# Optimization experiments

Measured on AMD Instinct MI355X. Metric: run time of the kernel, lower is better.

The kernel has to match this reference:

```python
import jax, jax.numpy as jnp
import numpy as np
from jax import lax

B, L_IN, D, D_INNER = 4, 1024, 512, 512
H, DK = 8, 64
WIN = [4, 4, 4]
INNER_SIZE = 5   # temporal intra-level neighborhood size
SEM_K = 32       # opt.semantic_node: topk per level for semantic mask
N_LAYER = 2


def _build_temporal_mask(input_size, window_size, inner_size):
    # faithful port of Encoder.get_mask (Pyraformer-Naive mask)
    all_size = [input_size]
    for w in window_size:
        all_size.append(all_size[-1] // w)
    L = sum(all_size)
    m = np.zeros((L, L), dtype=np.float32)
    iw = inner_size // 2
    starts = [sum(all_size[:i]) for i in range(len(all_size))]
    for li, n in enumerate(all_size):
        st = starts[li]
        for i in range(st, st + n):
            m[i, max(i - iw, st):min(i + iw + 1, st + n)] = 1
    for li in range(1, len(all_size)):
        st = starts[li]
        prev = all_size[li - 1]
        w = window_size[li - 1]
        for i in range(st, st + all_size[li]):
            ls = st - prev + (i - st) * w
            rs = st if i == st + all_size[li] - 1 else st - prev + (i - st + 1) * w
            m[i, ls:rs] = 1
            m[ls:rs, i] = 1
    return (1 - m).astype(bool), all_size

TMASK_NP, ALL_SIZE = _build_temporal_mask(L_IN, WIN, INNER_SIZE)
L_TOT = sum(ALL_SIZE)  # 1360


def _ln(x, g, b, eps):
    mu = jnp.mean(x, axis=-1, keepdims=True)
    var = jnp.mean(jnp.square(x - mu), axis=-1, keepdims=True)
    return (x - mu) * lax.rsqrt(var + eps) * g + b


def _mha(x, Wq, Wk, Wv, fcW, fcb, g, b, mask):
    # post-norm MHA (normalize_before=False), dropout disabled (eval)
    Bq, L, _ = x.shape
    q = (x @ Wq).reshape(Bq, L, H, DK)
    k = (x @ Wk).reshape(Bq, L, H, DK)
    v = (x @ Wv).reshape(Bq, L, H, DK)
    a = jnp.einsum('bqhd,bkhd->bhqk', q, k) / np.float32(DK ** 0.5)
    a = jnp.where(mask, -jnp.inf, a)
    p = jax.nn.softmax(a, axis=-1)
    o = jnp.einsum('bhqk,bkhd->bqhd', p, v).reshape(Bq, L, H * DK)
    return _ln(o @ fcW + fcb + x, g, b, 1e-6)


def _semantic_mask(x):
    # get_semantic_mask: per-level cosine similarity, mask topk-most-similar within each level
    nrm = jnp.linalg.norm(x, axis=-1, keepdims=True)
    xn = x / jnp.maximum(nrm, 1e-8)
    sim = jnp.einsum('bid,bjd->bij', xn, xn)
    Bq = x.shape[0]
    mask = jnp.zeros((Bq, L_TOT, L_TOT), dtype=bool)
    bidx = jnp.arange(Bq)[:, None, None]
    start = 0
    for n in ALL_SIZE:
        k = min(n, SEM_K)
        blk = sim[:, start:start + n, start:start + n]
        idx = lax.top_k(blk, k)[1]              # [B, n, k]
        ridx = jnp.arange(n)[None, :, None]
        bm = jnp.zeros((Bq, n, n), dtype=bool).at[bidx, ridx, idx].set(True)
        mask = mask.at[:, start:start + n, start:start + n].set(bm)
        start += n
    return mask


def _bottleneck(x, dW, db, cW, cb, uW, ub, g, b):
    t = jnp.transpose(x @ dW + db, (0, 2, 1))  # [B, d_inner, L]
    outs = []
    for i in range(len(WIN)):
        t = lax.conv_general_dilated(t, cW[i], (WIN[i],), 'VALID',
                                     dimension_numbers=('NCH', 'OIH', 'NCH')) + cb[i][None, :, None]
        t = t / np.float32(np.sqrt(1.0 + 1e-5))  # eval BatchNorm with identity running stats
        t = jax.nn.elu(t)
        outs.append(t)
    pyr = jnp.transpose(jnp.concatenate(outs, axis=2), (0, 2, 1)) @ uW + ub
    return _ln(jnp.concatenate([x, pyr], axis=1), g, b, 1e-5)


def _forward(x_enc, down_W, down_b, conv_W, conv_b, up_W, up_b, bc_ln_g, bc_ln_b,
             attn_Wq, attn_Wk, attn_Wv, attn_fcW, attn_fcb, attn_ln_g, attn_ln_b,
             ffn_W1, ffn_b1, ffn_W2, ffn_b2, ffn_ln_g, ffn_ln_b):
    tmask = jnp.asarray(TMASK_NP)[None, None]  # [1,1,Lt,Lt]
    x = _bottleneck(x_enc, down_W, down_b, conv_W, conv_b, up_W, up_b, bc_ln_g, bc_ln_b)
    for l in range(N_LAYER):
        res = x
        t_out = _mha(x, attn_Wq[l, 0], attn_Wk[l, 0], attn_Wv[l, 0], attn_fcW[l, 0],
                     attn_fcb[l, 0], attn_ln_g[l, 0], attn_ln_b[l, 0], tmask)
        smask = _semantic_mask(x)[:, None]     # [B,1,Lt,Lt]
        s_out = _mha(x, attn_Wq[l, 1], attn_Wk[l, 1], attn_Wv[l, 1], attn_fcW[l, 1],
                     attn_fcb[l, 1], attn_ln_g[l, 1], attn_ln_b[l, 1], smask)
        x = (t_out + s_out + res) / 3.0
        res = x
        h = jax.nn.relu(x @ ffn_W1[l] + ffn_b1[l])
        x = _ln(h @ ffn_W2[l] + ffn_b2[l] + res, ffn_ln_g[l], ffn_ln_b[l], 1e-6)
    return x


def setup_inputs() -> dict:
    key = jax.random.key(0)
    ks = jax.random.split(key, 16)
    s = 0.02
    inp = {
        'x_enc': jax.random.normal(ks[0], (B, L_IN, D), jnp.float32),
        'down_W': jax.random.normal(ks[1], (D, D_INNER), jnp.float32) * s,
        'down_b': jnp.zeros((D_INNER,), jnp.float32),
        'conv_W': jax.random.normal(ks[2], (3, D_INNER, D_INNER, WIN[0]), jnp.float32) * s,
        'conv_b': jnp.zeros((3, D_INNER), jnp.float32),
        'up_W': jax.random.normal(ks[3], (D_INNER, D), jnp.float32) * s,
        'up_b': jnp.zeros((D,), jnp.float32),
        'bc_ln_g': jnp.ones((D,), jnp.float32),
        'bc_ln_b': jnp.zeros((D,), jnp.float32),
        'attn_Wq': jax.random.normal(ks[4], (N_LAYER, 2, D, H * DK), jnp.float32) * s,
        'attn_Wk': jax.random.normal(ks[5], (N_LAYER, 2, D, H * DK), jnp.float32) * s,
        'attn_Wv': jax.random.normal(ks[6], (N_LAYER, 2, D, H * DK), jnp.float32) * s,
        'attn_fcW': jax.random.normal(ks[7], (N_LAYER, 2, H * DK, D), jnp.float32) * s,
        'attn_fcb': jnp.zeros((N_LAYER, 2, D), jnp.float32),
        'attn_ln_g': jnp.ones((N_LAYER, 2, D), jnp.float32),
        'attn_ln_b': jnp.zeros((N_LAYER, 2, D), jnp.float32),
        'ffn_W1': jax.random.normal(ks[8], (N_LAYER, D, D_INNER), jnp.float32) * s,
        'ffn_b1': jnp.zeros((N_LAYER, D_INNER), jnp.float32),
        'ffn_W2': jax.random.normal(ks[9], (N_LAYER, D_INNER, D), jnp.float32) * s,
        'ffn_b2': jnp.zeros((N_LAYER, D), jnp.float32),
        'ffn_ln_g': jnp.ones((N_LAYER, D), jnp.float32),
        'ffn_ln_b': jnp.zeros((N_LAYER, D), jnp.float32),
    }
    return inp


def reference(x_enc, down_W, down_b, conv_W, conv_b, up_W, up_b, bc_ln_g, bc_ln_b,
              attn_Wq, attn_Wk, attn_Wv, attn_fcW, attn_fcb, attn_ln_g, attn_ln_b,
              ffn_W1, ffn_b1, ffn_W2, ffn_b2, ffn_ln_g, ffn_ln_b):
    return _forward(x_enc, down_W, down_b, conv_W, conv_b, up_W, up_b, bc_ln_g, bc_ln_b,
                    attn_Wq, attn_Wk, attn_Wv, attn_fcW, attn_fcb, attn_ln_g, attn_ln_b,
                    ffn_W1, ffn_b1, ffn_W2, ffn_b2, ffn_ln_g, ffn_ln_b)
```

## Files before the change

kernel.cpp:

```cpp
#include <hip/hip_runtime.h>
#include <float.h>
#include <math.h>
#include <stdint.h>

#define LT 1360
#define BB 4
#define DM 512
#define NHH 8
#define NBLE 2785280
#define MBW 24
#define QSCALE 0.18033688f

typedef __attribute__((ext_vector_type(8))) short short8;
typedef __attribute__((ext_vector_type(4))) float f32x4;
typedef unsigned long long u64;

__device__ __forceinline__ ushort f2b(float x){
    uint32_t u = __float_as_uint(x);
    return (ushort)((u + 0x7fffu + ((u >> 16) & 1u)) >> 16);
}
__device__ __forceinline__ float b2f(ushort u){
    return __uint_as_float(((uint32_t)u) << 16);
}
__device__ __forceinline__ float ex2(float x){
    float r;
    asm("v_exp_f32 %0, %1" : "=v"(r) : "v"(x));
    return r;
}
__device__ __forceinline__ uint32_t pkbf(float lo, float hi){
    uint32_t r;
    asm("v_cvt_pk_bf16_f32 %0, %1, %2" : "=v"(r) : "v"(lo), "v"(hi));
    return r;
}

#define SG0 0
#define SG1 1048576
#define SG2 (SG1 + 65536)
#define SG3 (SG2 + 4096)
#define SBT (SG3 + 256)

__device__ __forceinline__ void blk_info(int i, int& bi, int& st, int& n){
    if (i < 1024){ bi = 0; st = 0;    n = 1024; }
    else if (i < 1280){ bi = 1; st = 1024; n = 256; }
    else if (i < 1344){ bi = 2; st = 1280; n = 64; }
    else { bi = 3; st = 1344; n = 16; }
}

__global__ __launch_bounds__(256)
void build_tidx(int* __restrict__ idx, int* __restrict__ cnt){
    int i = blockIdx.x * 256 + threadIdx.x;
    if (i >= LT) return;
    int bi, st, n; blk_info(i, bi, st, n);
    int c = 0; int* row = idx + i * 12;
    int lo = (i - 2 > st) ? i - 2 : st;
    int hi = (i + 2 < st + n - 1) ? i + 2 : st + n - 1;
    for (int j = lo; j <= hi; j++) row[c++] = j;
    if (bi < 3) row[c++] = st + n + (i - st) / 4;
    if (bi > 0){
        int stc = st - n * 4;
        int base = stc + (i - st) * 4;
        for (int t = 0; t < 4; t++) row[c++] = base + t;
    }
    cnt[i] = c;
    for (int t = c; t < 12; t++) row[t] = 0;
}

__global__ __launch_bounds__(256)
void wtrans(const float* __restrict__ W, ushort* __restrict__ Wt, int K, int N, long dstStride){
    int mat = blockIdx.z;
    const float* Ws = W + (size_t)mat * K * N;
    ushort* Wd = Wt + (size_t)mat * dstStride;
    int k0 = blockIdx.y << 6, n0 = blockIdx.x << 6;
    __shared__ ushort t[64][72];
    int tid = threadIdx.x;
    #pragma unroll
    for (int p = 0; p < 4; p++){
        int idx = tid + (p << 8);
        int r = idx >> 4, c4 = (idx & 15) << 2;
        float4 v = *(const float4*)(Ws + (size_t)(k0 + r) * N + n0 + c4);
        t[c4+0][r] = f2b(v.x); t[c4+1][r] = f2b(v.y);
        t[c4+2][r] = f2b(v.z); t[c4+3][r] = f2b(v.w);
    }
    __syncthreads();
    #pragma unroll
    for (int p = 0; p < 4; p++){
        int idx = tid + (p << 8);
        int r = idx >> 4, c4 = (idx & 15) << 2;
        *(uint2*)&Wd[(size_t)(n0 + r) * K + k0 + c4] = *(uint2*)&t[r][c4];
    }
}

__global__ __launch_bounds__(256)
void wconv(const float* __restrict__ cw, ushort* __restrict__ wt){
    int conv = blockIdx.y;
// ... 447 lines not shown
    *(uint4*)&Bl[srow][sc8] = vbl;
    __syncthreads();
    for (int k0 = 0; k0 < 512; k0 += 32){
        bool nx = (k0 + 32 < 512);
        if (nx){
            vah = *(const uint4*)(pAh + k0 + 32);
            val = *(const uint4*)(pAl + k0 + 32);
            vbh = *(const uint4*)(pBh + k0 + 32);
            vbl = *(const uint4*)(pBl + k0 + 32);
        }
        __builtin_amdgcn_s_setprio(1);
        short8 ah0 = *(const short8*)&Ah[wr + l15][quad << 3];
        short8 ah1 = *(const short8*)&Ah[wr + 16 + l15][quad << 3];
        short8 al0 = *(const short8*)&Al[wr + l15][quad << 3];
        short8 al1 = *(const short8*)&Al[wr + 16 + l15][quad << 3];
        short8 bh0 = *(const short8*)&Bh[wc + l15][quad << 3];
        short8 bh1 = *(const short8*)&Bh[wc + 16 + l15][quad << 3];
        short8 bl0 = *(const short8*)&Bl[wc + l15][quad << 3];
        short8 bl1 = *(const short8*)&Bl[wc + 16 + l15][quad << 3];
        acc[0][0] = __builtin_amdgcn_mfma_f32_16x16x32_bf16(ah0, bh0, acc[0][0], 0, 0, 0);
        acc[0][0] = __builtin_amdgcn_mfma_f32_16x16x32_bf16(ah0, bl0, acc[0][0], 0, 0, 0);
        acc[0][0] = __builtin_amdgcn_mfma_f32_16x16x32_bf16(al0, bh0, acc[0][0], 0, 0, 0);
        acc[0][1] = __builtin_amdgcn_mfma_f32_16x16x32_bf16(ah0, bh1, acc[0][1], 0, 0, 0);
        acc[0][1] = __builtin_amdgcn_mfma_f32_16x16x32_bf16(ah0, bl1, acc[0][1], 0, 0, 0);
        acc[0][1] = __builtin_amdgcn_mfma_f32_16x16x32_bf16(al0, bh1, acc[0][1], 0, 0, 0);
        acc[1][0] = __builtin_amdgcn_mfma_f32_16x16x32_bf16(ah1, bh0, acc[1][0], 0, 0, 0);
        acc[1][0] = __builtin_amdgcn_mfma_f32_16x16x32_bf16(ah1, bl0, acc[1][0], 0, 0, 0);
        acc[1][0] = __builtin_amdgcn_mfma_f32_16x16x32_bf16(al1, bh0, acc[1][0], 0, 0, 0);
        acc[1][1] = __builtin_amdgcn_mfma_f32_16x16x32_bf16(ah1, bh1, acc[1][1], 0, 0, 0);
        acc[1][1] = __builtin_amdgcn_mfma_f32_16x16x32_bf16(ah1, bl1, acc[1][1], 0, 0, 0);
        acc[1][1] = __builtin_amdgcn_mfma_f32_16x16x32_bf16(al1, bh1, acc[1][1], 0, 0, 0);
        __builtin_amdgcn_s_setprio(0);
        if (nx){
            __syncthreads();
            *(uint4*)&Ah[srow][sc8] = vah;
            *(uint4*)&Al[srow][sc8] = val;
            *(uint4*)&Bh[srow][sc8] = vbh;
            *(uint4*)&Bl[srow][sc8] = vbl;
            __syncthreads();
        }
    }
    #pragma unroll
    for (int mi = 0; mi < 2; mi++){
        #pragma unroll
        for (int r = 0; r < 4; r++){
            int row = gm + wr + (mi << 4) + (quad << 2) + r;
            if (row < n){
                #pragma unroll
                for (int ni = 0; ni < 2; ni++){
                    int col = gn + wc + (ni << 4) + l15;
                    if (col < n) Cb[(size_t)row * n + col] = acc[mi][ni][r];
                }
            }
        }
    }
}

__global__ __launch_bounds__(256)
void pcat_copy(const float* __restrict__ C1, const float* __restrict__ C2,
               const float* __restrict__ C3, float* __restrict__ PC){
    int idx = blockIdx.x * 256 + threadIdx.x;
    int d = idx & 511;
    int r = (idx >> 9) % 336;
    int b = idx / (336 * 512);
    float v;
    if (r < 256)       v = C1[(((size_t)b * 256 + r) << 9) + d];
    else if (r < 320)  v = C2[(((size_t)b * 64 + (r - 256)) << 9) + d];
    else               v = C3[(((size_t)b * 16 + (r - 320)) << 9) + d];
    PC[idx] = v;
}

__global__ __launch_bounds__(256)
void xenc_copy(const float* __restrict__ xe, float* __restrict__ dst){
    int idx = blockIdx.x * 256 + threadIdx.x;
    int d = idx & 511;
    int l = (idx >> 9) & 1023;
    int b = idx >> 19;
    dst[(((size_t)b * LT + l) << 9) + d] = xe[idx];
}

__global__ __launch_bounds__(256)
void ln_kernel(const float* __restrict__ in, const float* __restrict__ g,
               const float* __restrict__ bta, float* __restrict__ out,
               ushort* __restrict__ ob, float eps){
    int wid = threadIdx.x >> 6, lane = threadIdx.x & 63;
    int row = blockIdx.x * 4 + wid;
    const float* p = in + ((size_t)row << 9);
    float vals[8]; float s = 0.f, s2 = 0.f;
    #pragma unroll
    for (int t = 0; t < 8; t++){
        float v = p[lane + t * 64]; vals[t] = v; s += v; s2 += v * v;
    }
    #pragma unroll
    for (int off = 32; off; off >>= 1){
        s  += __shfl_xor(s,  off, 64);
        s2 += __shfl_xor(s2, off, 64);
    }
    float mu = s * (1.f / 512.f);
    float var = s2 * (1.f / 512.f) - mu * mu;
    float r = rsqrtf(var + eps);
    float* q = out + ((size_t)row << 9);
    ushort* qb = ob ? ob + ((size_t)row << 9) : nullptr;
    #pragma unroll
    for (int t = 0; t < 8; t++){
        int c = lane + t * 64;
        float v = (vals[t] - mu) * r * g[c] + bta[c];
        q[c] = v;
        if (qb) qb[c] = f2b(v);
    }
}

__global__ __launch_bounds__(256)
void ln2_add3(const float* __restrict__ in0, const float* __restrict__ in1,
              const float* __restrict__ g0, const float* __restrict__ b0,
              const float* __restrict__ g1, const float* __restrict__ b1,
              float* __restrict__ X, ushort* __restrict__ ob, float eps){
    int wid = threadIdx.x >> 6, lane = threadIdx.x & 63;
    int row = blockIdx.x * 4 + wid;
    const float* p0 = in0 + ((size_t)row << 9);
    const float* p1 = in1 + ((size_t)row << 9);
    float v0[8], v1[8];
    float s0 = 0.f, q0 = 0.f, s1 = 0.f, q1 = 0.f;
    #pragma unroll
    for (int t = 0; t < 8; t++){
        float a = p0[lane + t * 64]; v0[t] = a; s0 += a; q0 += a * a;
        float c = p1[lane + t * 64]; v1[t] = c; s1 += c; q1 += c * c;
    }
    #pragma unroll
    for (int off = 32; off; off >>= 1){
        s0 += __shfl_xor(s0, off, 64);
        q0 += __shfl_xor(q0, off, 64);
        s1 += __shfl_xor(s1, off, 64);
        q1 += __shfl_xor(q1, off, 64);
    }
    float mu0 = s0 * (1.f / 512.f);
    float r0 = rsqrtf(q0 * (1.f / 512.f) - mu0 * mu0 + eps);
    float mu1 = s1 * (1.f / 512.f);
    float r1 = rsqrtf(q1 * (1.f / 512.f) - mu1 * mu1 + eps);
    float* xp = X + ((size_t)row << 9);
    ushort* qb = ob + ((size_t)row << 9);
    #pragma unroll
    for (int t = 0; t < 8; t++){
        int c = lane + t * 64;
        float sn0 = (v0[t] - mu0) * r0 * g0[c] + b0[c];
        float sn1 = (v1[t] - mu1) * r1 * g1[c] + b1[c];
        float nv = (sn0 + sn1 + xp[c]) * (1.f / 3.f);
        xp[c] = nv;
        qb[c] = f2b(nv);
    }
}

__global__ __launch_bounds__(256)
void rownorm_kernel(const float* __restrict__ in, ushort* __restrict__ XHp,
                    ushort* __restrict__ XLp){
    int wid = threadIdx.x >> 6, lane = threadIdx.x & 63;
    int row = blockIdx.x * 4 + wid;
    const float* p = in + ((size_t)row << 9);
    float vals[8]; float s2 = 0.f;
    #pragma unroll
    for (int t = 0; t < 8; t++){
        float v = p[lane + t * 64]; vals[t] = v; s2 += v * v;
    }
    #pragma unroll
    for (int off = 32; off; off >>= 1) s2 += __shfl_xor(s2, off, 64);
    float inv = 1.f / fmaxf(sqrtf(s2), 1e-8f);
    ushort* qh = XHp + ((size_t)row << 9);
    ushort* ql = XLp + ((size_t)row << 9);
    #pragma unroll
    for (int t = 0; t < 8; t++){
        float v = vals[t] * inv;
        ushort h = f2b(v);
        qh[lane + t * 64] = h;
        ql[lane + t * 64] = f2b(v - b2f(h));
    }
}

__global__ __launch_bounds__(256)
void topk_sel(const float* __restrict__ SIM, u64* __restrict__ MB){
    int wid = threadIdx.x >> 6, lane = threadIdx.x & 63;
    int r = blockIdx.x * 4 + wid;
    int b = r / LT, i = r % LT;
    int bi, st, n; blk_info(i, bi, st, n);
    u64* mrow = MB + ((size_t)b * LT + i) * MBW;
    if (n == 16){
        u64 myw = 0;
        if (lane == 21) myw = ~0ULL;
        if (lane < MBW) mrow[lane] = myw;
        return;
    }
    int goff = (bi == 0) ? SG0 : (bi == 1) ? SG1 : SG2;
    const float* srow = SIM + (size_t)b * SBT + goff + (size_t)(i - st) * n;
    int ns = n >> 6;
    float vals[16];
    #pragma unroll
    for (int t = 0; t < 16; t++)
        vals[t] = (t < ns) ? srow[lane + (t << 6)] : -FLT_MAX;

    float c[32];
    #pragma unroll
    for (int t = 0; t < 16; t++) c[t] = vals[t];
    #pragma unroll
    for (int k = 2; k <= 16; k <<= 1){
        #pragma unroll
        for (int j = k >> 1; j > 0; j >>= 1){
            #pragma unroll
            for (int t = 0; t < 16; t++){
                int l = t ^ j;
                if (l > t){
                    float lo = fminf(c[t], c[l]);
                    float hi = fmaxf(c[t], c[l]);
                    if ((t & k) == 0){ c[t] = hi; c[l] = lo; }
                    else             { c[t] = lo; c[l] = hi; }
                }
            }
        }
    }
    #pragma unroll
    for (int t = 16; t < 32; t++) c[t] = -FLT_MAX;

    float V32;
    #pragma unroll
    for (int rd = 0; rd < 6; rd++){
        float f[32];
        #pragma unroll
        for (int t = 0; t < 32; t++) f[t] = __shfl_xor(c[t], 1 << rd, 64);
        float m[32];
        #pragma unroll
        for (int t = 0; t < 32; t++) m[t] = fmaxf(c[t], f[31 - t]);
        if (rd < 5){
            #pragma unroll
            for (int d = 16; d >= 1; d >>= 1){
                #pragma unroll
                for (int t = 0; t < 32; t++){
                    if ((t & d) == 0){
                        float lo = fminf(m[t], m[t + d]);
                        m[t] = fmaxf(m[t], m[t + d]);
                        m[t + d] = lo;
                    }
                }
            }
            #pragma unroll
            for (int t = 0; t < 32; t++) c[t] = m[t];
        } else {
            float mn = m[0];
            #pragma unroll
            for (int t = 1; t < 32; t++) mn = fminf(mn, m[t]);
            V32 = mn;
        }
    }

    int cnt_gt = 0;
    #pragma unroll
    for (int t = 0; t < 16; t++){
        u64 bg = __ballot(vals[t] > V32);
        cnt_gt += __popcll(bg);
    }
    int need = 32 - cnt_gt;
    u64 lmask = (1ULL << lane) - 1;
    u64 myw = 0;
    if (lane == 21) myw = 0xFFFFFFFFFFFF0000ULL;
    int eqrun = 0;
    int w0 = st >> 6;
    #pragma unroll
    for (int t = 0; t < 16; t++){
        bool eq = (vals[t] == V32);
        u64 beq = __ballot(eq);
        int below = __popcll(beq & lmask);
        bool sel = (vals[t] > V32) || (eq && (eqrun + below) < need);
        eqrun += __popcll(beq);
        u64 wsel = __ballot(sel);
        if (t < ns && lane == w0 + t) myw = wsel;
    }
    if (lane < MBW) mrow[lane] = myw;
}

__global__ __launch_bounds__(256)
void attn_sparse(const ushort* __restrict__ Q, const ushort* __restrict__ Kp,
                 const ushort* __restrict__ Vn, const int* __restrict__ IDX,
                 const int* __restrict__ CNT, ushort* __restrict__ O){
    int wid = threadIdx.x >> 6, lane = threadIdx.x & 63;
    int row = blockIdx.x * 4 + wid;
    int b = row / (NHH * LT);
    int rem = row % (NHH * LT);
    int h = rem / LT, i = rem % LT;
    int c = CNT[i];
    int jl = IDX[i * 12 + (lane % 12)];
    float qd = b2f(Q[(((size_t)b * LT + i) << 9) + h * 64 + lane]);
    const ushort* kb = Kp + (((size_t)b * LT) << 9) + h * 64 + lane;
    const ushort* vb = Vn + (((size_t)b * LT) << 9) + h * 64 + lane;
    int jj[12];
    #pragma unroll
    for (int t = 0; t < 12; t++) jj[t] = __shfl(jl, t, 64);
    float kv[12], vv[12];
    #pragma unroll
    for (int t = 0; t < 12; t++){
        kv[t] = b2f(kb[(size_t)jj[t] << 9]);
        vv[t] = b2f(vb[(size_t)jj[t] << 9]);
    }
    float lsum = 0.f, o = 0.f;
    #pragma unroll
    for (int t = 0; t < 12; t++){
        float s = qd * kv[t];
        #pragma unroll
        for (int off = 32; off; off >>= 1) s += __shfl_xor(s, off, 64);
        float p = (t < c) ? exp2f(s) : 0.f;
        lsum += p;
        o += p * vv[t];
    }
    O[(((size_t)b * LT + i) << 9) + h * 64 + lane] = f2b(o / lsum);
}

__global__ __launch_bounds__(256)
void flash_mfma(const ushort* __restrict__ Q, const ushort* __restrict__ Kp,
                const ushort* __restrict__ Vt, const u64* __restrict__ MB,
                ushort* __restrict__ AO)
{
    __shared__ ushort Ks[2][64][76];
    __shared__ ushort Vs[2][64][76];
    int bh = blockIdx.x, b = bh >> 3, h = bh & 7;
    int q0 = blockIdx.y << 6;
    int tid = threadIdx.x;
    int w = tid >> 6, lane = tid & 63, quad = lane >> 4, l15 = lane & 15;

    int qm = q0 + w * 16 + l15;
    int qmc = (qm < LT) ? qm : (LT - 1);
    const ushort* qp = Q + ((size_t)(b * LT + qmc) << 9) + h * 64 + (quad << 3);
    short8 qf0 = *(const short8*)qp;
    short8 qf1 = *(const short8*)(qp + 32);

    float l_part = 0.f;
    f32x4 Oacc[4];
    #pragma unroll
    for (int dt = 0; dt < 4; dt++) Oacc[dt] = (f32x4){0.f,0.f,0.f,0.f};

    int srow = tid >> 2, sc = (tid & 3) << 4;

    const ushort* kpp = Kp + ((size_t)(b * LT + srow) << 9) + h * 64 + sc;
    const ushort* vpp = Vt + (size_t)(b * 512 + h * 64 + srow) * LT + sc;
    const u64* mpp = MB + ((size_t)b * LT + qmc) * MBW;

    int srcA = ((quad & 1) << 5) + l15;
    int srcB = srcA + 16;
    bool ntHi = (quad & 2) != 0;

    {
        uint4 k0v = *(const uint4*)kpp;
        uint4 k1v = *(const uint4*)(kpp + 8);
        uint4 v0v = *(const uint4*)vpp;
        uint4 v1v = *(const uint4*)(vpp + 8);
        kpp += 64 * 512; vpp += 64;
        *(uint4*)&Ks[0][srow][sc]     = k0v;
        *(uint4*)&Ks[0][srow][sc + 8] = k1v;
        *(uint4*)&Vs[0][srow][sc]     = v0v;
        *(uint4*)&Vs[0][srow][sc + 8] = v1v;
    }
    __syncthreads();

    for (int kt = 0; kt < 22; kt++){
        int cur = kt & 1;
        bool havenext = (kt + 1 < 22);
        uint4 kn0, kn1, vn0, vn1;
        if (havenext){
            kn0 = *(const uint4*)kpp;
            kn1 = *(const uint4*)(kpp + 8);
            vn0 = *(const uint4*)vpp;
            vn1 = *(const uint4*)(vpp + 8);
            kpp += 64 * 512; vpp += 64;
        }
        u64 mw = mpp[kt];
        f32x4 s[4];
        #pragma unroll
        for (int nt = 0; nt < 4; nt++) s[nt] = (f32x4){0.f,0.f,0.f,0.f};
        __builtin_amdgcn_s_setprio(1);
        #pragma unroll
        for (int nt = 0; nt < 4; nt++){
            short8 kf0 = *(const short8*)&Ks[cur][(nt << 4) + l15][quad << 3];
            short8 kf1 = *(const short8*)&Ks[cur][(nt << 4) + l15][32 + (quad << 3)];
            s[nt] = __builtin_amdgcn_mfma_f32_16x16x32_bf16(kf0, qf0, s[nt], 0, 0, 0);
            s[nt] = __builtin_amdgcn_mfma_f32_16x16x32_bf16(kf1, qf1, s[nt], 0, 0, 0);
        }
        __builtin_amdgcn_s_setprio(0);
        u64 msh = mw >> (quad << 2);
        uint32_t pk01[4], pk23[4];
        #pragma unroll
        for (int nt = 0; nt < 4; nt++){
            float p0 = ((uint32_t)(msh >> (nt * 16 + 0)) & 1u) ? 0.f : ex2(s[nt][0]);
            float p1 = ((uint32_t)(msh >> (nt * 16 + 1)) & 1u) ? 0.f : ex2(s[nt][1]);
            float p2 = ((uint32_t)(msh >> (nt * 16 + 2)) & 1u) ? 0.f : ex2(s[nt][2]);
            float p3 = ((uint32_t)(msh >> (nt * 16 + 3)) & 1u) ? 0.f : ex2(s[nt][3]);
            l_part += (p0 + p1) + (p2 + p3);
            pk01[nt] = pkbf(p0, p1);
            pk23[nt] = pkbf(p2, p3);
        }
        uint4 pa, pb;
        {
            uint32_t t0, t1;
            t0 = __shfl(pk01[0], srcA, 64); t1 = __shfl(pk01[1], srcA, 64);
            pa.x = ntHi ? t1 : t0;
            t0 = __shfl(pk23[0], srcA, 64); t1 = __shfl(pk23[1], srcA, 64);
            pa.y = ntHi ? t1 : t0;
            t0 = __shfl(pk01[0], srcB, 64); t1 = __shfl(pk01[1], srcB, 64);
            pa.z = ntHi ? t1 : t0;
            t0 = __shfl(pk23[0], srcB, 64); t1 = __shfl(pk23[1], srcB, 64);
            pa.w = ntHi ? t1 : t0;
            t0 = __shfl(pk01[2], srcA, 64); t1 = __shfl(pk01[3], srcA, 64);
            pb.x = ntHi ? t1 : t0;
            t0 = __shfl(pk23[2], srcA, 64); t1 = __shfl(pk23[3], srcA, 64);
            pb.y = ntHi ? t1 : t0;
            t0 = __shfl(pk01[2], srcB, 64); t1 = __shfl(pk01[3], srcB, 64);
            pb.z = ntHi ? t1 : t0;
            t0 = __shfl(pk23[2], srcB, 64); t1 = __shfl(pk23[3], srcB, 64);
            pb.w = ntHi ? t1 : t0;
        }
        short8 pf0 = *(const short8*)&pa;
        short8 pf1 = *(const short8*)&pb;
        __builtin_amdgcn_s_setprio(1);
        #pragma unroll
        for (int dt = 0; dt < 4; dt++){
            short8 vf0 = *(const short8*)&Vs[cur][(dt << 4) + l15][quad << 3];
            short8 vf1 = *(const short8*)&Vs[cur][(dt << 4) + l15][32 + (quad << 3)];
            Oacc[dt] = __builtin_amdgcn_mfma_f32_16x16x32_bf16(pf0, vf0, Oacc[dt], 0, 0, 0);
            Oacc[dt] = __builtin_amdgcn_mfma_f32_16x16x32_bf16(pf1, vf1, Oacc[dt], 0, 0, 0);
        }
        __builtin_amdgcn_s_setprio(0);
        if (havenext){
            int nb = cur ^ 1;
            *(uint4*)&Ks[nb][srow][sc]     = kn0;
            *(uint4*)&Ks[nb][srow][sc + 8] = kn1;
            *(uint4*)&Vs[nb][srow][sc]     = vn0;
            *(uint4*)&Vs[nb][srow][sc + 8] = vn1;
        }
        __syncthreads();
    }
    l_part += __shfl_xor(l_part, 16, 64);
    l_part += __shfl_xor(l_part, 32, 64);
    #pragma unroll
    for (int r = 0; r < 4; r++){
        int qrow = q0 + (w << 4) + (quad << 2) + r;
        if (qrow < LT){
            float lr = __shfl(l_part, (lane & 48) + (quad << 2) + r, 64);
            float inv = 1.f / lr;
            #pragma unroll
            for (int dt = 0; dt < 4; dt++)
                AO[((size_t)(b * LT + qrow) << 9) + h * 64 + (dt << 4) + l15] =
                    f2b(Oacc[dt][r] * inv);
        }
    }
}

extern "C" void kernel_launch(void* const* d_in, const int* in_sizes, int n_in,
                              void* d_out, int out_size, void* d_ws, size_t ws_size,
                              hipStream_t stream)
{
    const float* x_enc   = (const float*)d_in[0];
    const float* down_W  = (const float*)d_in[1];
    const float* down_b  = (const float*)d_in[2];
    const float* conv_W  = (const float*)d_in[3];
    const float* conv_b  = (const float*)d_in[4];
    const float* up_W    = (const float*)d_in[5];
    const float* up_b    = (const float*)d_in[6];
    const float* bc_g    = (const float*)d_in[7];
    const float* bc_b    = (const float*)d_in[8];
    const float* aWq     = (const float*)d_in[9];
    const float* aWk     = (const float*)d_in[10];
    const float* aWv     = (const float*)d_in[11];
    const float* afcW    = (const float*)d_in[12];
    const float* afcb    = (const float*)d_in[13];
    const float* alng    = (const float*)d_in[14];
    const float* alnb    = (const float*)d_in[15];
    const float* fW1     = (const float*)d_in[16];
    const float* fb1     = (const float*)d_in[17];
    const float* fW2     = (const float*)d_in[18];
    const float* fb2     = (const float*)d_in[19];
    const float* flng    = (const float*)d_in[20];
    const float* flnb    = (const float*)d_in[21];

    const size_t NBL = (size_t)NBLE;
    float* X   = (float*)d_ws;
    float* TMP = X   + NBL;
    float* Qb  = TMP + NBL;
    float* Kb  = Qb  + NBL;
    float* Vb  = Kb  + NBL;
    float* AO  = Vb  + NBL;
    float* TO  = AO  + NBL;
    float* SO  = TO  + NBL;
    u64* MBm = (u64*)(SO + NBL);
    int* TIDX = (int*)(MBm + (size_t)BB * LT * MBW);
    int* TCNT = TIDX + (size_t)LT * 12;
    ushort* WG = (ushort*)(TCNT + LT);
    const size_t M512 = 262144;
    ushort* WdownT = WG;                 size_t wo = M512;
    ushort* WupT   = WG + wo;            wo += M512;
    ushort* Wqkv   = WG + wo;            wo += 12 * M512;
    ushort* WfT    = WG + wo;            wo += 4 * M512;
    ushort* W1T    = WG + wo;            wo += 2 * M512;
    ushort* W2T    = WG + wo;            wo += 2 * M512;
    ushort* WCt    = WG + wo;            wo += 3 * 1048576;
    float* LP = (float*)(WG + wo);
    (void)LP;
    size_t need = 8 * NBL * sizeof(float) + (size_t)BB * LT * MBW * 8
                + (size_t)LT * 13 * 4 + wo * sizeof(ushort)
                + (size_t)2 * BB * NHH * LT * 4;
    if (ws_size < need) return;

    float* Y    = Qb;
    float* C1   = Kb;
    float* C2   = C1 + (size_t)BB*256*512;
    float* C3   = C2 + (size_t)BB*64*512;
    float* PCAT = Vb;
    float* SKP  = AO;
    ushort* XNh = (ushort*)AO;
    ushort* XNl = XNh + NBLE;
    float* SIMB = Qb;
    ushort* U   = (ushort*)Qb;
    ushort* XB  = (ushort*)SO;
    ushort* AOb0 = (ushort*)AO;
    ushort* AOb1 = AOb0 + NBLE;
    ushort* HfB = (ushort*)Qb;
    float* TMP1 = TO;

    auto gemmN = [&](const void* A, int abf, const ushort* Bw, const float* bias,
                     const float* res, void* C, int M,
                     int act, int omode, int mpb, int orpb, int ooff){
        dim3 grid(8, M / 64);
        if (abf) gemm64t<1><<<grid, 256, 0, stream>>>(A, Bw, bias, res, C, M, 512, 512,
                                                      act, omode, mpb, orpb, ooff);
        else     gemm64t<0><<<grid, 256, 0, stream>>>(A, Bw, bias, res, C, M, 512, 512,
                                                      act, omode, mpb, orpb, ooff);
    };
    auto convG = [&](const float* A, const ushort* Bw, const float* bias,
                     float* C, int M){
        const int S = 8, K = 2048, N = 512;
        gemm_sk<<<dim3(8, M / 64, S), 256, 0, stream>>>(A, Bw, SKP, M, N, K, K / S);
        sk_reduce<<<(M * N) / 1024, 256, 0, stream>>>(SKP, bias, C, M * N, S);
    };

    build_tidx<<<(LT + 255) / 256, 256, 0, stream>>>(TIDX, TCNT);
    wtrans<<<dim3(8, 8, 1), 256, 0, stream>>>(down_W, WdownT, 512, 512, M512);
    wtrans<<<dim3(8, 8, 1), 256, 0, stream>>>(up_W,   WupT,   512, 512, M512);
    wtrans<<<dim3(8, 8, 4), 256, 0, stream>>>(aWq,  Wqkv + 0 * M512, 512, 512, 3 * (long)M512);
    wtrans<<<dim3(8, 8, 4), 256, 0, stream>>>(aWk,  Wqkv + 1 * M512, 512, 512, 3 * (long)M512);
    wtrans<<<dim3(8, 8, 4), 256, 0, stream>>>(aWv,  Wqkv + 2 * M512, 512, 512, 3 * (long)M512);
    wtrans<<<dim3(8, 8, 4), 256, 0, stream>>>(afcW, WfT, 512, 512, M512);
    wtrans<<<dim3(8, 8, 2), 256, 0, stream>>>(fW1,  W1T, 512, 512, M512);
    wtrans<<<dim3(8, 8, 2), 256, 0, stream>>>(fW2,  W2T, 512, 512, M512);
    wconv<<<dim3(4096, 3), 256, 0, stream>>>(conv_W, WCt);

    gemmN(x_enc, 0, WdownT, down_b, nullptr, Y, BB*1024, 0, 0, 0, 0, 0);
    convG(Y,  WCt,             conv_b + 0,    C1, BB*256);
    convG(C1, WCt + 1048576,   conv_b + 512,  C2, BB*64);
    convG(C2, WCt + 2*1048576, conv_b + 1024, C3, BB*16);
    pcat_copy<<<(BB*336*512)/256, 256, 0, stream>>>(C1, C2, C3, PCAT);
    gemmN(PCAT, 0, WupT, up_b, nullptr, TMP, BB*336, 0, 0, 336, LT, 1024);
    xenc_copy<<<(BB*1024*512)/256, 256, 0, stream>>>(x_enc, TMP);
    ln_kernel<<<(BB*LT)/4, 256, 0, stream>>>(TMP, bc_g, bc_b, X, XB, 1e-5f);

    for (int l = 0; l < 2; l++){
        rownorm_kernel<<<(BB*LT)/4, 256, 0, stream>>>(X, XNh, XNl);
        sim_mfma<<<dim3(274, BB), 256, 0, stream>>>(XNh, XNl, SIMB);
        topk_sel<<<(BB*LT)/4, 256, 0, stream>>>(SIMB, MBm);

        gemm_qkv<<<dim3(24, 85), 256, 0, stream>>>(XB, Wqkv + (size_t)l * 6 * M512,
                                                   U, BB*LT, 3072, 512);
        attn_sparse<<<(BB*NHH*LT)/4, 256, 0, stream>>>(U, U + 2*NBL, U + 5*NBL,
                                                       TIDX, TCNT, AOb0);
        flash_mfma<<<dim3(32, 22), 256, 0, stream>>>(U + NBL, U + 3*NBL, U + 4*NBL,
                                                     MBm, AOb1);
        gemm_fc2<<<dim3(8, 85, 2), 256, 0, stream>>>(AOb0, AOb1,
            WfT + (size_t)(2*l) * M512, WfT + (size_t)(2*l + 1) * M512,
            afcb + (size_t)(2*l) * 512, afcb + (size_t)(2*l + 1) * 512,
            X, TMP, TMP1, BB*LT, 512, 512);
        ln2_add3<<<(BB*LT)/4, 256, 0, stream>>>(TMP, TMP1,
            alng + (size_t)(2*l) * 512, alnb + (size_t)(2*l) * 512,
            alng + (size_t)(2*l + 1) * 512, alnb + (size_t)(2*l + 1) * 512,
            X, XB, 1e-6f);

        gemmN(XB,  1, W1T + (size_t)l * M512, fb1 + (size_t)l*512, nullptr, HfB, BB*LT, 2, 1, 0, 0, 0);
        gemmN(HfB, 1, W2T + (size_t)l * M512, fb2 + (size_t)l*512, X, TMP, BB*LT, 0, 0, 0, 0, 0);
        ln_kernel<<<(BB*LT)/4, 256, 0, stream>>>(TMP, flng + (size_t)l*512, flnb + (size_t)l*512,
                                                 (l == 1) ? (float*)d_out : X,
                                                 (l == 1) ? nullptr : XB, 1e-6f);
    }
}
```

Measured before the change: 732.9 us.

## Fuse row-normalization into LayerNorm and merge two attention kernels into one launch

The cosine-similarity row normalization (bf16 hi/lo split) moves into the preceding LayerNorm kernel, so the separate rownorm pass, with its extra full read of X, goes away. The sparse temporal attention and the masked flash attention become one kernel whose blocks branch on blockIdx, so both branches run concurrently in a single launch. In exchange, every block of the merged kernel reserves the flash branch's shared-memory tiles, which may lower occupancy for the lightweight sparse blocks.

```diff
diff --git a/kernel.cpp b/kernel.cpp
--- a/kernel.cpp
+++ b/kernel.cpp
@@ -10,6 +10,7 @@
 #define NBLE 2785280
 #define MBW 24
 #define QSCALE 0.18033688f
+#define NFLASH 704
 
 typedef __attribute__((ext_vector_type(8))) short short8;
 typedef __attribute__((ext_vector_type(4))) float f32x4;
@@ -623,7 +624,8 @@
 __global__ __launch_bounds__(256)
 void ln_kernel(const float* __restrict__ in, const float* __restrict__ g,
                const float* __restrict__ bta, float* __restrict__ out,
-               ushort* __restrict__ ob, float eps){
+               ushort* __restrict__ ob, ushort* __restrict__ xh,
+               ushort* __restrict__ xl, float eps){
     int wid = threadIdx.x >> 6, lane = threadIdx.x & 63;
     int row = blockIdx.x * 4 + wid;
     const float* p = in + ((size_t)row << 9);
@@ -642,12 +644,28 @@
     float r = rsqrtf(var + eps);
     float* q = out + ((size_t)row << 9);
     ushort* qb = ob ? ob + ((size_t)row << 9) : nullptr;
+    float nv[8]; float sn2 = 0.f;
     #pragma unroll
     for (int t = 0; t < 8; t++){
         int c = lane + t * 64;
         float v = (vals[t] - mu) * r * g[c] + bta[c];
         q[c] = v;
         if (qb) qb[c] = f2b(v);
+        nv[t] = v; sn2 += v * v;
+    }
+    if (xh){
+        #pragma unroll
+        for (int off = 32; off; off >>= 1) sn2 += __shfl_xor(sn2, off, 64);
+        float inv = 1.f / fmaxf(sqrtf(sn2), 1e-8f);
+        ushort* qh = xh + ((size_t)row << 9);
+        ushort* ql = xl + ((size_t)row << 9);
+        #pragma unroll
+        for (int t = 0; t < 8; t++){
+            float v = nv[t] * inv;
+            ushort h = f2b(v);
+            qh[lane + t * 64] = h;
+            ql[lane + t * 64] = f2b(v - b2f(h));
+        }
     }
 }
 
@@ -688,31 +706,6 @@
         float nv = (sn0 + sn1 + xp[c]) * (1.f / 3.f);
         xp[c] = nv;
         qb[c] = f2b(nv);
-    }
-}
-
-__global__ __launch_bounds__(256)
-void rownorm_kernel(const float* __restrict__ in, ushort* __restrict__ XHp,
-                    ushort* __restrict__ XLp){
-    int wid = threadIdx.x >> 6, lane = threadIdx.x & 63;
-    int row = blockIdx.x * 4 + wid;
-    const float* p = in + ((size_t)row << 9);
-    float vals[8]; float s2 = 0.f;
-    #pragma unroll
-    for (int t = 0; t < 8; t++){
-        float v = p[lane + t * 64]; vals[t] = v; s2 += v * v;
-    }
-    #pragma unroll
-    for (int off = 32; off; off >>= 1) s2 += __shfl_xor(s2, off, 64);
-    float inv = 1.f / fmaxf(sqrtf(s2), 1e-8f);
-    ushort* qh = XHp + ((size_t)row << 9);
-    ushort* ql = XLp + ((size_t)row << 9);
-    #pragma unroll
-    for (int t = 0; t < 8; t++){
-        float v = vals[t] * inv;
-        ushort h = f2b(v);
-        qh[lane + t * 64] = h;
-        ql[lane + t * 64] = f2b(v - b2f(h));
     }
 }
 
@@ -816,176 +809,180 @@
 }
 
 __global__ __launch_bounds__(256)
-void attn_sparse(const ushort* __restrict__ Q, const ushort* __restrict__ Kp,
-                 const ushort* __restrict__ Vn, const int* __restrict__ IDX,
-                 const int* __restrict__ CNT, ushort* __restrict__ O){
-    int wid = threadIdx.x >> 6, lane = threadIdx.x & 63;
-    int row = blockIdx.x * 4 + wid;
-    int b = row / (NHH * LT);
-    int rem = row % (NHH * LT);
-    int h = rem / LT, i = rem % LT;
-    int c = CNT[i];
-    int jl = IDX[i * 12 + (lane % 12)];
-    float qd = b2f(Q[(((size_t)b * LT + i) << 9) + h * 64 + lane]);
-    const ushort* kb = Kp + (((size_t)b * LT) << 9) + h * 64 + lane;
-    const ushort* vb = Vn + (((size_t)b * LT) << 9) + h * 64 + lane;
-    int jj[12];
-    #pragma unroll
-    for (int t = 0; t < 12; t++) jj[t] = __shfl(jl, t, 64);
-    float kv[12], vv[12];
-    #pragma unroll
-    for (int t = 0; t < 12; t++){
-        kv[t] = b2f(kb[(size_t)jj[t] << 9]);
-        vv[t] = b2f(vb[(size_t)jj[t] << 9]);
-    }
-    float lsum = 0.f, o = 0.f;
-    #pragma unroll
-    for (int t = 0; t < 12; t++){
-        float s = qd * kv[t];
-        #pragma unroll
-        for (int off = 32; off; off >>= 1) s += __shfl_xor(s, off, 64);
-        float p = (t < c) ? exp2f(s) : 0.f;
-        lsum += p;
-        o += p * vv[t];
-    }
-    O[(((size_t)b * LT + i) << 9) + h * 64 + lane] = f2b(o / lsum);
-}
-
-__global__ __launch_bounds__(256)
-void flash_mfma(const ushort* __restrict__ Q, const ushort* __restrict__ Kp,
-                const ushort* __restrict__ Vt, const u64* __restrict__ MB,
-                ushort* __restrict__ AO)
+void attn_fused(const ushort* __restrict__ U, const u64* __restrict__ MB,
+                const int* __restrict__ IDX, const int* __restrict__ CNT,
+                ushort* __restrict__ AO0, ushort* __restrict__ AO1)
 {
     __shared__ ushort Ks[2][64][76];
     __shared__ ushort Vs[2][64][76];
-    int bh = blockIdx.x, b = bh >> 3, h = bh & 7;
-    int q0 = blockIdx.y << 6;
-    int tid = threadIdx.x;
-    int w = tid >> 6, lane = tid & 63, quad = lane >> 4, l15 = lane & 15;
-
-    int qm = q0 + w * 16 + l15;
-    int qmc = (qm < LT) ? qm : (LT - 1);
-    const ushort* qp = Q + ((size_t)(b * LT + qmc) << 9) + h * 64 + (quad << 3);
-    short8 qf0 = *(const short8*)qp;
-    short8 qf1 = *(const short8*)(qp + 32);
-
-    float l_part = 0.f;
-    f32x4 Oacc[4];
-    #pragma unroll
-    for (int dt = 0; dt < 4; dt++) Oacc[dt] = (f32x4){0.f,0.f,0.f,0.f};
-
-    int srow = tid >> 2, sc = (tid & 3) << 4;
-
-    const ushort* kpp = Kp + ((size_t)(b * LT + srow) << 9) + h * 64 + sc;
-    const ushort* vpp = Vt + (size_t)(b * 512 + h * 64 + srow) * LT + sc;
-    const u64* mpp = MB + ((size_t)b * LT + qmc) * MBW;
-
-    int srcA = ((quad & 1) << 5) + l15;
-    int srcB = srcA + 16;
-    bool ntHi = (quad & 2) != 0;
-
-    {
-        uint4 k0v = *(const uint4*)kpp;
-        uint4 k1v = *(const uint4*)(kpp + 8);
-        uint4 v0v = *(const uint4*)vpp;
-        uint4 v1v = *(const uint4*)(vpp + 8);
-        kpp += 64 * 512; vpp += 64;
-        *(uint4*)&Ks[0][srow][sc]     = k0v;
-        *(uint4*)&Ks[0][srow][sc + 8] = k1v;
-        *(uint4*)&Vs[0][srow][sc]     = v0v;
-        *(uint4*)&Vs[0][srow][sc + 8] = v1v;
-    }
-    __syncthreads();
-
-    for (int kt = 0; kt < 22; kt++){
-        int cur = kt & 1;
-        bool havenext = (kt + 1 < 22);
-        uint4 kn0, kn1, vn0, vn1;
-        if (havenext){
-            kn0 = *(const uint4*)kpp;
-            kn1 = *(const uint4*)(kpp + 8);
-            vn0 = *(const uint4*)vpp;
-            vn1 = *(const uint4*)(vpp + 8);
+    if (blockIdx.x < NFLASH){
+        const ushort* Q  = U + (size_t)NBLE;
+        const ushort* Kp = U + (size_t)3*NBLE;
+        const ushort* Vt = U + (size_t)4*NBLE;
+        int fid = blockIdx.x;
+        int bh = fid & 31, b = bh >> 3, h = bh & 7;
+        int q0 = (fid >> 5) << 6;
+        int tid = threadIdx.x;
+        int w = tid >> 6, lane = tid & 63, quad = lane >> 4, l15 = lane & 15;
+
+        int qm = q0 + w * 16 + l15;
+        int qmc = (qm < LT) ? qm : (LT - 1);
+        const ushort* qp = Q + ((size_t)(b * LT + qmc) << 9) + h * 64 + (quad << 3);
+        short8 qf0 = *(const short8*)qp;
+        short8 qf1 = *(const short8*)(qp + 32);
+
+        float l_part = 0.f;
+        f32x4 Oacc[4];
+        #pragma unroll
+        for (int dt = 0; dt < 4; dt++) Oacc[dt] = (f32x4){0.f,0.f,0.f,0.f};
+
+        int srow = tid >> 2, sc = (tid & 3) << 4;
+
+        const ushort* kpp = Kp + ((size_t)(b * LT + srow) << 9) + h * 64 + sc;
+        const ushort* vpp = Vt + (size_t)(b * 512 + h * 64 + srow) * LT + sc;
+        const u64* mpp = MB + ((size_t)b * LT + qmc) * MBW;
+
+        int srcA = ((quad & 1) << 5) + l15;
+        int srcB = srcA + 16;
+        bool ntHi = (quad & 2) != 0;
+
+        {
+            uint4 k0v = *(const uint4*)kpp;
+            uint4 k1v = *(const uint4*)(kpp + 8);
+            uint4 v0v = *(const uint4*)vpp;
+            uint4 v1v = *(const uint4*)(vpp + 8);
             kpp += 64 * 512; vpp += 64;
-        }
-        u64 mw = mpp[kt];
-        f32x4 s[4];
-        #pragma unroll
-        for (int nt = 0; nt < 4; nt++) s[nt] = (f32x4){0.f,0.f,0.f,0.f};
-        __builtin_amdgcn_s_setprio(1);
-        #pragma unroll
-        for (int nt = 0; nt < 4; nt++){
-            short8 kf0 = *(const short8*)&Ks[cur][(nt << 4) + l15][quad << 3];
-            short8 kf1 = *(const short8*)&Ks[cur][(nt << 4) + l15][32 + (quad << 3)];
-            s[nt] = __builtin_amdgcn_mfma_f32_16x16x32_bf16(kf0, qf0, s[nt], 0, 0, 0);
-            s[nt] = __builtin_amdgcn_mfma_f32_16x16x32_bf16(kf1, qf1, s[nt], 0, 0, 0);
-        }
-        __builtin_amdgcn_s_setprio(0);
-        u64 msh = mw >> (quad << 2);
-        uint32_t pk01[4], pk23[4];
-        #pragma unroll
-        for (int nt = 0; nt < 4; nt++){
-            float p0 = ((uint32_t)(msh >> (nt * 16 + 0)) & 1u) ? 0.f : ex2(s[nt][0]);
-            float p1 = ((uint32_t)(msh >> (nt * 16 + 1)) & 1u) ? 0.f : ex2(s[nt][1]);
-            float p2 = ((uint32_t)(msh >> (nt * 16 + 2)) & 1u) ? 0.f : ex2(s[nt][2]);
-            float p3 = ((uint32_t)(msh >> (nt * 16 + 3)) & 1u) ? 0.f : ex2(s[nt][3]);
-            l_part += (p0 + p1) + (p2 + p3);
-            pk01[nt] = pkbf(p0, p1);
-            pk23[nt] = pkbf(p2, p3);
-        }
-        uint4 pa, pb;
-        {
-            uint32_t t0, t1;
-            t0 = __shfl(pk01[0], srcA, 64); t1 = __shfl(pk01[1], srcA, 64);
-            pa.x = ntHi ? t1 : t0;
-            t0 = __shfl(pk23[0], srcA, 64); t1 = __shfl(pk23[1], srcA, 64);
-            pa.y = ntHi ? t1 : t0;
-            t0 = __shfl(pk01[0], srcB, 64); t1 = __shfl(pk01[1], srcB, 64);
-            pa.z = ntHi ? t1 : t0;
-            t0 = __shfl(pk23[0], srcB, 64); t1 = __shfl(pk23[1], srcB, 64);
-            pa.w = ntHi ? t1 : t0;
-            t0 = __shfl(pk01[2], srcA, 64); t1 = __shfl(pk01[3], srcA, 64);
-            pb.x = ntHi ? t1 : t0;
-            t0 = __shfl(pk23[2], srcA, 64); t1 = __shfl(pk23[3], srcA, 64);
-            pb.y = ntHi ? t1 : t0;
-            t0 = __shfl(pk01[2], srcB, 64); t1 = __shfl(pk01[3], srcB, 64);
-            pb.z = ntHi ? t1 : t0;
-            t0 = __shfl(pk23[2], srcB, 64); t1 = __shfl(pk23[3], srcB, 64);
-            pb.w = ntHi ? t1 : t0;
-        }
-        short8 pf0 = *(const short8*)&pa;
-        short8 pf1 = *(const short8*)&pb;
-        __builtin_amdgcn_s_setprio(1);
-        #pragma unroll
-        for (int dt = 0; dt < 4; dt++){
-            short8 vf0 = *(const short8*)&Vs[cur][(dt << 4) + l15][quad << 3];
-            short8 vf1 = *(const short8*)&Vs[cur][(dt << 4) + l15][32 + (quad << 3)];
-            Oacc[dt] = __builtin_amdgcn_mfma_f32_16x16x32_bf16(pf0, vf0, Oacc[dt], 0, 0, 0);
-            Oacc[dt] = __builtin_amdgcn_mfma_f32_16x16x32_bf16(pf1, vf1, Oacc[dt], 0, 0, 0);
-        }
-        __builtin_amdgcn_s_setprio(0);
-        if (havenext){
-            int nb = cur ^ 1;
-            *(uint4*)&Ks[nb][srow][sc]     = kn0;
-            *(uint4*)&Ks[nb][srow][sc + 8] = kn1;
-            *(uint4*)&Vs[nb][srow][sc]     = vn0;
-            *(uint4*)&Vs[nb][srow][sc + 8] = vn1;
+            *(uint4*)&Ks[0][srow][sc]     = k0v;
+            *(uint4*)&Ks[0][srow][sc + 8] = k1v;
+            *(uint4*)&Vs[0][srow][sc]     = v0v;
+            *(uint4*)&Vs[0][srow][sc + 8] = v1v;
         }
         __syncthreads();
-    }
-    l_part += __shfl_xor(l_part, 16, 64);
-    l_part += __shfl_xor(l_part, 32, 64);
-    #pragma unroll
-    for (int r = 0; r < 4; r++){
-        int qrow = q0 + (w << 4) + (quad << 2) + r;
-        if (qrow < LT){
-            float lr = __shfl(l_part, (lane & 48) + (quad << 2) + r, 64);
-            float inv = 1.f / lr;
-            #pragma unroll
-            for (int dt = 0; dt < 4; dt++)
-                AO[((size_t)(b * LT + qrow) << 9) + h * 64 + (dt << 4) + l15] =
-                    f2b(Oacc[dt][r] * inv);
-        }
+
+        for (int kt = 0; kt < 22; kt++){
+            int cur = kt & 1;
+            bool havenext = (kt + 1 < 22);
+            uint4 kn0, kn1, vn0, vn1;
+            if (havenext){
+                kn0 = *(const uint4*)kpp;
+                kn1 = *(const uint4*)(kpp + 8);
+                vn0 = *(const uint4*)vpp;
+                vn1 = *(const uint4*)(vpp + 8);
+                kpp += 64 * 512; vpp += 64;
+            }
+            u64 mw = mpp[kt];
+            f32x4 s[4];
+            #pragma unroll
+            for (int nt = 0; nt < 4; nt++) s[nt] = (f32x4){0.f,0.f,0.f,0.f};
+            __builtin_amdgcn_s_setprio(1);
+            #pragma unroll
+            for (int nt = 0; nt < 4; nt++){
+                short8 kf0 = *(const short8*)&Ks[cur][(nt << 4) + l15][quad << 3];
+                short8 kf1 = *(const short8*)&Ks[cur][(nt << 4) + l15][32 + (quad << 3)];
+                s[nt] = __builtin_amdgcn_mfma_f32_16x16x32_bf16(kf0, qf0, s[nt], 0, 0, 0);
+                s[nt] = __builtin_amdgcn_mfma_f32_16x16x32_bf16(kf1, qf1, s[nt], 0, 0, 0);
+            }
+            __builtin_amdgcn_s_setprio(0);
+            u64 msh = mw >> (quad << 2);
+            uint32_t pk01[4], pk23[4];
+            #pragma unroll
+            for (int nt = 0; nt < 4; nt++){
+                float p0 = ((uint32_t)(msh >> (nt * 16 + 0)) & 1u) ? 0.f : ex2(s[nt][0]);
+                float p1 = ((uint32_t)(msh >> (nt * 16 + 1)) & 1u) ? 0.f : ex2(s[nt][1]);
+                float p2 = ((uint32_t)(msh >> (nt * 16 + 2)) & 1u) ? 0.f : ex2(s[nt][2]);
+                float p3 = ((uint32_t)(msh >> (nt * 16 + 3)) & 1u) ? 0.f : ex2(s[nt][3]);
+                l_part += (p0 + p1) + (p2 + p3);
+                pk01[nt] = pkbf(p0, p1);
+                pk23[nt] = pkbf(p2, p3);
+            }
+            uint4 pa, pb;
+            {
+                uint32_t t0, t1;
+                t0 = __shfl(pk01[0], srcA, 64); t1 = __shfl(pk01[1], srcA, 64);
+                pa.x = ntHi ? t1 : t0;
+                t0 = __shfl(pk23[0], srcA, 64); t1 = __shfl(pk23[1], srcA, 64);
+                pa.y = ntHi ? t1 : t0;
+                t0 = __shfl(pk01[0], srcB, 64); t1 = __shfl(pk01[1], srcB, 64);
+                pa.z = ntHi ? t1 : t0;
+                t0 = __shfl(pk23[0], srcB, 64); t1 = __shfl(pk23[1], srcB, 64);
+                pa.w = ntHi ? t1 : t0;
+                t0 = __shfl(pk01[2], srcA, 64); t1 = __shfl(pk01[3], srcA, 64);
+                pb.x = ntHi ? t1 : t0;
+                t0 = __shfl(pk23[2], srcA, 64); t1 = __shfl(pk23[3], srcA, 64);
+                pb.y = ntHi ? t1 : t0;
+                t0 = __shfl(pk01[2], srcB, 64); t1 = __shfl(pk01[3], srcB, 64);
+                pb.z = ntHi ? t1 : t0;
+                t0 = __shfl(pk23[2], srcB, 64); t1 = __shfl(pk23[3], srcB, 64);
+                pb.w = ntHi ? t1 : t0;
+            }
+            short8 pf0 = *(const short8*)&pa;
+            short8 pf1 = *(const short8*)&pb;
+            __builtin_amdgcn_s_setprio(1);
+            #pragma unroll
+            for (int dt = 0; dt < 4; dt++){
+                short8 vf0 = *(const short8*)&Vs[cur][(dt << 4) + l15][quad << 3];
+                short8 vf1 = *(const short8*)&Vs[cur][(dt << 4) + l15][32 + (quad << 3)];
+                Oacc[dt] = __builtin_amdgcn_mfma_f32_16x16x32_bf16(pf0, vf0, Oacc[dt], 0, 0, 0);
+                Oacc[dt] = __builtin_amdgcn_mfma_f32_16x16x32_bf16(pf1, vf1, Oacc[dt], 0, 0, 0);
+            }
+            __builtin_amdgcn_s_setprio(0);
+            if (havenext){
+                int nb = cur ^ 1;
+                *(uint4*)&Ks[nb][srow][sc]     = kn0;
+                *(uint4*)&Ks[nb][srow][sc + 8] = kn1;
+                *(uint4*)&Vs[nb][srow][sc]     = vn0;
+                *(uint4*)&Vs[nb][srow][sc + 8] = vn1;
+            }
+            __syncthreads();
+        }
+        l_part += __shfl_xor(l_part, 16, 64);
+        l_part += __shfl_xor(l_part, 32, 64);
+        #pragma unroll
+        for (int r = 0; r < 4; r++){
+            int qrow = q0 + (w << 4) + (quad << 2) + r;
+            if (qrow < LT){
+                float lr = __shfl(l_part, (lane & 48) + (quad << 2) + r, 64);
+                float inv = 1.f / lr;
+                #pragma unroll
+                for (int dt = 0; dt < 4; dt++)
+                    AO1[((size_t)(b * LT + qrow) << 9) + h * 64 + (dt << 4) + l15] =
+                        f2b(Oacc[dt][r] * inv);
+            }
+        }
+    } else {
+        const ushort* Q  = U;
+        const ushort* Kp = U + (size_t)2*NBLE;
+        const ushort* Vn = U + (size_t)5*NBLE;
+        int wid = threadIdx.x >> 6, lane = threadIdx.x & 63;
+        int row = (blockIdx.x - NFLASH) * 4 + wid;
+        int b = row / (NHH * LT);
+        int rem = row % (NHH * LT);
+        int h = rem / LT, i = rem % LT;
+        int c = CNT[i];
+        int jl = IDX[i * 12 + (lane % 12)];
+        float qd = b2f(Q[(((size_t)b * LT + i) << 9) + h * 64 + lane]);
+        const ushort* kb = Kp + (((size_t)b * LT) << 9) + h * 64 + lane;
+        const ushort* vb = Vn + (((size_t)b * LT) << 9) + h * 64 + lane;
+        int jj[12];
+        #pragma unroll
+        for (int t = 0; t < 12; t++) jj[t] = __shfl(jl, t, 64);
+        float kv[12], vv[12];
+        #pragma unroll
+        for (int t = 0; t < 12; t++){
+            kv[t] = b2f(kb[(size_t)jj[t] << 9]);
+            vv[t] = b2f(vb[(size_t)jj[t] << 9]);
+        }
+        float lsum = 0.f, o = 0.f;
+        #pragma unroll
+        for (int t = 0; t < 12; t++){
+            float s = qd * kv[t];
+            #pragma unroll
+            for (int off = 32; off; off >>= 1) s += __shfl_xor(s, off, 64);
+            float p = (t < c) ? exp2f(s) : 0.f;
+            lsum += p;
+            o += p * vv[t];
+        }
+        AO0[(((size_t)b * LT + i) << 9) + h * 64 + lane] = f2b(o / lsum);
     }
 }
 
@@ -1094,19 +1091,16 @@
     pcat_copy<<<(BB*336*512)/256, 256, 0, stream>>>(C1, C2, C3, PCAT);
     gemmN(PCAT, 0, WupT, up_b, nullptr, TMP, BB*336, 0, 0, 336, LT, 1024);
     xenc_copy<<<(BB*1024*512)/256, 256, 0, stream>>>(x_enc, TMP);
-    ln_kernel<<<(BB*LT)/4, 256, 0, stream>>>(TMP, bc_g, bc_b, X, XB, 1e-5f);
+    ln_kernel<<<(BB*LT)/4, 256, 0, stream>>>(TMP, bc_g, bc_b, X, XB, XNh, XNl, 1e-5f);
 
     for (int l = 0; l < 2; l++){
-        rownorm_kernel<<<(BB*LT)/4, 256, 0, stream>>>(X, XNh, XNl);
         sim_mfma<<<dim3(274, BB), 256, 0, stream>>>(XNh, XNl, SIMB);
         topk_sel<<<(BB*LT)/4, 256, 0, stream>>>(SIMB, MBm);
 
         gemm_qkv<<<dim3(24, 85), 256, 0, stream>>>(XB, Wqkv + (size_t)l * 6 * M512,
                                                    U, BB*LT, 3072, 512);
-        attn_sparse<<<(BB*NHH*LT)/4, 256, 0, stream>>>(U, U + 2*NBL, U + 5*NBL,
-                                                       TIDX, TCNT, AOb0);
-        flash_mfma<<<dim3(32, 22), 256, 0, stream>>>(U + NBL, U + 3*NBL, U + 4*NBL,
-                                                     MBm, AOb1);
+        attn_fused<<<dim3(NFLASH + (BB*NHH*LT)/4), 256, 0, stream>>>(
+            U, MBm, TIDX, TCNT, AOb0, AOb1);
         gemm_fc2<<<dim3(8, 85, 2), 256, 0, stream>>>(AOb0, AOb1,
             WfT + (size_t)(2*l) * M512, WfT + (size_t)(2*l + 1) * M512,
             afcb + (size_t)(2*l) * 512, afcb + (size_t)(2*l + 1) * 512,
@@ -1120,6 +1114,8 @@
         gemmN(HfB, 1, W2T + (size_t)l * M512, fb2 + (size_t)l*512, X, TMP, BB*LT, 0, 0, 0, 0, 0);
         ln_kernel<<<(BB*LT)/4, 256, 0, stream>>>(TMP, flng + (size_t)l*512, flnb + (size_t)l*512,
                                                  (l == 1) ? (float*)d_out : X,
-                                                 (l == 1) ? nullptr : XB, 1e-6f);
-    }
-}
+                                                 (l == 1) ? nullptr : XB,
+                                                 (l == 1) ? nullptr : XNh,
+                                                 (l == 1) ? nullptr : XNl, 1e-6f);
+    }
+}
```

Measured after the change: 703.6 us. -4.0%, faster.
